# Performance work log

Measured on AMD Instinct MI355X. Metric: run time of the kernel, lower is better.

The kernel has to match this reference:

```python
import jax, jax.numpy as jnp
import numpy as np

N_NODES = 100000
N_EDGES = 1600000
IN_DIM = 64
HIDDEN_DIM = 64


def setup_inputs() -> dict:
    key = jax.random.key(0)
    ks = jax.random.split(key, 8)
    x = jax.random.normal(ks[0], (N_NODES, IN_DIM), dtype=jnp.float32)
    edge_index = jax.random.randint(ks[1], (2, N_EDGES), 0, N_NODES, dtype=jnp.int32)
    s = 1.0 / np.sqrt(IN_DIM)
    sh = 1.0 / np.sqrt(HIDDEN_DIM)
    # SAGEConv params: lin_l (applied to mean-aggregated neighbors, with bias),
    # lin_r (applied to root/self features, no bias) -- PyG defaults.
    w1l = jax.random.uniform(ks[2], (IN_DIM, HIDDEN_DIM), jnp.float32, -s, s)
    b1l = jax.random.uniform(ks[3], (HIDDEN_DIM,), jnp.float32, -s, s)
    w1r = jax.random.uniform(ks[4], (IN_DIM, HIDDEN_DIM), jnp.float32, -s, s)
    w2l = jax.random.uniform(ks[5], (HIDDEN_DIM, HIDDEN_DIM), jnp.float32, -sh, sh)
    b2l = jax.random.uniform(ks[6], (HIDDEN_DIM,), jnp.float32, -sh, sh)
    w2r = jax.random.uniform(ks[7], (HIDDEN_DIM, HIDDEN_DIM), jnp.float32, -sh, sh)
    return {"x": x, "edge_index": edge_index, "w1l": w1l, "b1l": b1l,
            "w1r": w1r, "w2l": w2l, "b2l": b2l, "w2r": w2r}


def reference(x, edge_index, w1l, b1l, w1r, w2l, b2l, w2r):
    n = x.shape[0]
    src, dst = edge_index[0], edge_index[1]
    # in-degree (number of incoming messages per target node), clamped to 1
    deg = jax.ops.segment_sum(jnp.ones(src.shape, x.dtype), dst, num_segments=n)
    inv_deg = 1.0 / jnp.maximum(deg, 1.0)  # [N]

    def sage_conv(h, wl, bl, wr):
        # mean aggregation of neighbor messages: scatter-add then normalize
        agg = jax.ops.segment_sum(h[src], dst, num_segments=n) * inv_deg[:, None]
        return agg @ wl + bl + h @ wr

    h = jax.nn.relu(sage_conv(x, w1l, b1l, w1r))  # conv1 + relu
    return sage_conv(h, w2l, b2l, w2r)            # conv2 (no activation)
```

## Files before the change

### kernel.cpp

```cpp
#include <hip/hip_runtime.h>
#include <hip/hip_fp16.h>


#define DIM 64
#define BN 64
#define MAXBUCK 2048
#define CHUNK 8192
#define GCAP 2048
#define GEMM_SMEM 12608

__device__ inline void fma4(float4& acc, float s, const float4 w) {
    acc.x = fmaf(s, w.x, acc.x); acc.y = fmaf(s, w.y, acc.y);
    acc.z = fmaf(s, w.z, acc.z); acc.w = fmaf(s, w.w, acc.w);
}

__device__ inline void addh8(float* acc, float4 raw) {
    const __half2* hp = (const __half2*)&raw;
#pragma unroll
    for (int k = 0; k < 4; ++k) {
        float2 f = __half22float2(hp[k]);
        acc[2 * k]     += f.x;
        acc[2 * k + 1] += f.y;
    }
}

__global__ __launch_bounds__(256) void prehist_kernel(const int* __restrict__ dst,
                                                      int* __restrict__ ghist,
                                                      int nE, int nbuck) {
    __shared__ int hist[MAXBUCK];
    const int t = threadIdx.x;
    for (int k = t; k < nbuck; k += 256) hist[k] = 0;
    __syncthreads();
    const int base = blockIdx.x * CHUNK;
    const int end = min(nE, base + CHUNK);
    for (int i = base + t; i < end; i += 256)
        atomicAdd(&hist[dst[i] >> 6], 1);
    __syncthreads();
    for (int k = t; k < nbuck; k += 256)
        if (hist[k]) atomicAdd(&ghist[k], hist[k]);
}

__global__ __launch_bounds__(1024) void scan_kernel(const int* __restrict__ ghist,
                                                    int* __restrict__ boff,
                                                    int* __restrict__ gcur, int nbuck) {
    __shared__ int sa[2048], sb[2048];
    const int t = threadIdx.x;
    int v0 = (t < nbuck) ? ghist[t] : 0;
    int v1 = (t + 1024 < nbuck) ? ghist[t + 1024] : 0;
    sa[t] = v0; sa[t + 1024] = v1;
    __syncthreads();
    int* in = sa; int* out = sb;
    for (int d = 1; d < 2048; d <<= 1) {
        out[t] = in[t] + ((t >= d) ? in[t - d] : 0);
        int i2 = t + 1024;
        out[i2] = in[i2] + ((i2 >= d) ? in[i2 - d] : 0);
        __syncthreads();
        int* tmp = in; in = out; out = tmp;
    }
    if (t < nbuck) { int e = in[t] - v0; boff[t] = e; gcur[t] = e; }
    if (t + 1024 < nbuck) { int e = in[t + 1024] - v1; boff[t + 1024] = e; gcur[t + 1024] = e; }
    if (t == 0) boff[nbuck] = in[2047];
}

__device__ inline void stage_rows(float* hs, const float* H, int base, int n, int t) {
    for (int p = 0; p < 4; ++p) {
        int idx = t + p * 256;
        int r = idx >> 4, c4 = idx & 15;
        int row = base + r;
        if (row < n)
            *(float4*)&hs[r * 68 + c4 * 4] = *(const float4*)&H[(size_t)row * 64 + c4 * 4];
    }
}
__device__ inline void stage_rows(float* hs, const __half* H, int base, int n, int t) {
    for (int p = 0; p < 2; ++p) {
        int idx = t + p * 256;
        int r = idx >> 3, c8 = idx & 7;
        int row = base + r;
        if (row < n) {
            float4 raw = *(const float4*)&H[(size_t)row * 64 + c8 * 8];
            const __half2* hp = (const __half2*)&raw;
            float2 f0 = __half22float2(hp[0]);
            float2 f1 = __half22float2(hp[1]);
            float2 f2 = __half22float2(hp[2]);
            float2 f3 = __half22float2(hp[3]);
            float* d = &hs[r * 68 + c8 * 8];
            *(float4*)d       = make_float4(f0.x, f0.y, f1.x, f1.y);
            *(float4*)(d + 4) = make_float4(f2.x, f2.y, f3.x, f3.y);
        }
    }
}

template <typename InT>
__device__ void gemm_body(int bid, float* smem,
                          const InT* __restrict__ H,
                          const float* __restrict__ Wl, const float* __restrict__ Wr,
                          const float* __restrict__ bias,
                          __half* __restrict__ A, __half* __restrict__ Dbuf, int n) {
    float* wsl = smem;
    float* wsr = smem + 4096;
    float* hs  = smem + 8192;
    float* bs  = smem + 8192 + 4352;
    const int t = threadIdx.x;
    for (int i = t * 4; i < 4096; i += 1024) {
        *(float4*)&wsl[i] = *(const float4*)&Wl[i];
        *(float4*)&wsr[i] = *(const float4*)&Wr[i];
    }
    if (t < 16) *(float4*)&bs[t * 4] = *(const float4*)&bias[t * 4];
    const int dg = t & 15;
    const int r0 = t >> 4;
    for (int ph = 0; ph < 2; ++ph) {
        const int base = bid * 128 + ph * 64;
        if (base >= n) break;
        __syncthreads();
        stage_rows(hs, H, base, n, t);
        __syncthreads();
        float4 accl[4] = {{0,0,0,0},{0,0,0,0},{0,0,0,0},{0,0,0,0}};
        float4 accr[4] = {{0,0,0,0},{0,0,0,0},{0,0,0,0},{0,0,0,0}};
#pragma unroll 4
        for (int kq = 0; kq < 16; ++kq) {
            float4 wl[4], wr[4];
#pragma unroll
            for (int i = 0; i < 4; ++i) {
                wl[i] = *(const float4*)&wsl[(kq * 4 + i) * 64 + dg * 4];
                wr[i] = *(const float4*)&wsr[(kq * 4 + i) * 64 + dg * 4];
            }
#pragma unroll
            for (int p = 0; p < 4; ++p) {
                float4 hv = *(const float4*)&hs[(r0 + p * 16) * 68 + kq * 4];
                fma4(accl[p], hv.x, wl[0]); fma4(accl[p], hv.y, wl[1]);
                fma4(accl[p], hv.z, wl[2]); fma4(accl[p], hv.w, wl[3]);
                fma4(accr[p], hv.x, wr[0]); fma4(accr[p], hv.y, wr[1]);
                fma4(accr[p], hv.z, wr[2]); fma4(accr[p], hv.w, wr[3]);
            }
        }
        float4 b4 = *(const float4*)&bs[dg * 4];
#pragma unroll
        for (int p = 0; p < 4; ++p) {
            int row = base + r0 + p * 16;
            if (row < n) {
                union { __half2 h[2]; float2 f; } u;
                u.h[0] = __floats2half2_rn(accl[p].x, accl[p].y);
                u.h[1] = __floats2half2_rn(accl[p].z, accl[p].w);
                *(float2*)&A[(size_t)row * 64 + dg * 4] = u.f;
                union { __half2 h[2]; float2 f; } v;
                v.h[0] = __floats2half2_rn(accr[p].x + b4.x, accr[p].y + b4.y);
                v.h[1] = __floats2half2_rn(accr[p].z + b4.z, accr[p].w + b4.w);
                *(float2*)&Dbuf[(size_t)row * 64 + dg * 4] = v.f;
            }
        }
    }
}

__global__ __launch_bounds__(256) void part_gemm_kernel(const int* __restrict__ src,
                                                        const int* __restrict__ dst,
                                                        int* __restrict__ gcur,
                                                        unsigned* __restrict__ P,
                                                        int nE, int nbuck, int pb,
                                                        const float* __restrict__ H,
                                                        const float* __restrict__ Wl,
                                                        const float* __restrict__ Wr,
                                                        const float* __restrict__ bias,
                                                        __half* __restrict__ A,
                                                        __half* __restrict__ Dbuf, int n) {
    __shared__ float smem[GEMM_SMEM];
    if ((int)blockIdx.x < pb) {
        int* hist = (int*)smem;
        const int t = threadIdx.x;
        for (int k = t; k < nbuck; k += 256) hist[k] = 0;
        __syncthreads();
        const int base = blockIdx.x * CHUNK;
        const int end = min(nE, base + CHUNK);
        for (int i = base + t; i < end; i += 256)
            atomicAdd(&hist[dst[i] >> 6], 1);
        __syncthreads();
        for (int k = t; k < nbuck; k += 256) {
            int h = hist[k];
            hist[k] = h ? atomicAdd(&gcur[k], h) : 0;
        }
        __syncthreads();
        for (int i = base + t; i < end; i += 256) {
            int d = dst[i];
            int bk = d >> 6;
            int pos = atomicAdd(&hist[bk], 1);
            P[pos] = ((unsigned)src[i] << 6) | (unsigned)(d & 63);
        }
    } else {
        gemm_body(blockIdx.x - pb, smem, H, Wl, Wr, bias, A, Dbuf, n);
    }
}

__global__ __launch_bounds__(256) void gemm_kernel(const __half* __restrict__ H,
                                                   const float* __restrict__ Wl,
                                                   const float* __restrict__ Wr,
                                                   const float* __restrict__ bias,
                                                   __half* __restrict__ A,
                                                   __half* __restrict__ Dbuf, int n) {
    __shared__ float smem[GEMM_SMEM];
    gemm_body(blockIdx.x, smem, H, Wl, Wr, bias, A, Dbuf, n);
}

template <bool RELU, typename OutT>
__global__ __launch_bounds__(256) void gather_sort_combine(const __half* __restrict__ A,
                                                           const __half* __restrict__ Dbuf,
                                                           const int* __restrict__ boff,
                                                           const unsigned* __restrict__ P,
                                                           int* __restrict__ spill,
                                                           OutT* __restrict__ out, int n) {
    __shared__ int hist[BN];
    __shared__ int rstart[BN];
    __shared__ int cur[BN];
    __shared__ int lsrc[GCAP];
    const int t = threadIdx.x;
    const int b = blockIdx.x;
    if (t < BN) hist[t] = 0;
    __syncthreads();
    const int start = boff[b], end = boff[b + 1];
    const int m = end - start;
    for (int i = start + t; i < end; i += 256)
        atomicAdd(&hist[P[i] & 63], 1);
    __syncthreads();
    if (t < 64) {
        int v = hist[t];
        int s = v;
#pragma unroll
        for (int d = 1; d < 64; d <<= 1) {
            int u = __shfl_up(s, d);
            if (t >= d) s += u;
        }
        rstart[t] = s - v;
        cur[t] = s - v;
    }
    __syncthreads();
    int* list = (m <= GCAP) ? (int*)lsrc : (spill + start);
    for (int i = start + t; i < end; i += 256) {
        unsigned p = P[i];
        int pos = atomicAdd(&cur[p & 63], 1);
        list[pos] = (int)(p >> 6);
    }
    __syncthreads();
    const int dg = t & 7;
    const size_t doff = (size_t)dg * 8;
    for (int pass = 0; pass < 2; ++pass) {
        const int r = pass * 32 + (t >> 3);
        const int node = b * BN + r;
        if (node >= n) continue;
        const int c = hist[r];
        const int* sp = list + rstart[r];
        float acc[8] = {0.f, 0.f, 0.f, 0.f, 0.f, 0.f, 0.f, 0.f};
        int j = 0;
        for (; j + 4 <= c; j += 4) {
            int e0 = sp[j + 0], e1 = sp[j + 1], e2 = sp[j + 2], e3 = sp[j + 3];
            float4 r0 = *(const float4*)&A[(size_t)e0 * 64 + doff];
            float4 r1 = *(const float4*)&A[(size_t)e1 * 64 + doff];
            float4 r2 = *(const float4*)&A[(size_t)e2 * 64 + doff];
            float4 r3 = *(const float4*)&A[(size_t)e3 * 64 + doff];
            addh8(acc, r0); addh8(acc, r1); addh8(acc, r2); addh8(acc, r3);
        }
        for (; j < c; ++j) {
            float4 rr = *(const float4*)&A[(size_t)sp[j] * 64 + doff];
            addh8(acc, rr);
        }
        const float inv = 1.0f / fmaxf((float)c, 1.0f);
        float d8[8] = {0,0,0,0,0,0,0,0};
        addh8(d8, *(const float4*)&Dbuf[(size_t)node * 64 + doff]);
        float o[8];
#pragma unroll
        for (int k = 0; k < 8; ++k) {
            float v = fmaf(acc[k], inv, d8[k]);
            o[k] = RELU ? fmaxf(v, 0.f) : v;
        }
        if constexpr (sizeof(OutT) == 2) {
            union { __half2 h[4]; float4 f; } u;
#pragma unroll
            for (int k = 0; k < 4; ++k)
                u.h[k] = __floats2half2_rn(o[2 * k], o[2 * k + 1]);
            *(float4*)&out[(size_t)node * 64 + doff] = u.f;
        } else {
            *(float4*)&out[(size_t)node * 64 + doff]     = make_float4(o[0], o[1], o[2], o[3]);
            *(float4*)&out[(size_t)node * 64 + doff + 4] = make_float4(o[4], o[5], o[6], o[7]);
        }
    }
}

extern "C" void kernel_launch(void* const* d_in, const int* in_sizes, int n_in,
                              void* d_out, int out_size, void* d_ws, size_t ws_size,
                              hipStream_t stream) {
    const float* x   = (const float*)d_in[0];
    const int*   ei  = (const int*)d_in[1];
    const float* w1l = (const float*)d_in[2];
    const float* b1l = (const float*)d_in[3];
    const float* w1r = (const float*)d_in[4];
    const float* w2l = (const float*)d_in[5];
    const float* b2l = (const float*)d_in[6];
    const float* w2r = (const float*)d_in[7];
    float* out = (float*)d_out;

    const int N = in_sizes[0] / DIM;
    const int E = in_sizes[1] / 2;
    const int* src = ei;
    const int* dst = ei + E;
    const int nbuck = (N + BN - 1) / BN;
    const int pb = (E + CHUNK - 1) / CHUNK;
    const int gb = (N + 127) / 128;

    int* ghist = (int*)d_ws;
    int* boff = ghist + nbuck;
    int* gcur = boff + nbuck + 1;
    unsigned* P = (unsigned*)(gcur + nbuck);
    int* spill = (int*)(P + E);
    uintptr_t ap = (uintptr_t)(spill + E);
    ap = (ap + 15) & ~(uintptr_t)15;
    __half* A  = (__half*)ap;
    __half* D  = A + (size_t)N * DIM;
    __half* h1 = D + (size_t)N * DIM;

    hipMemsetAsync(ghist, 0, nbuck * sizeof(int), stream);
    prehist_kernel<<<pb, 256, 0, stream>>>(dst, ghist, E, nbuck);
    scan_kernel<<<1, 1024, 0, stream>>>(ghist, boff, gcur, nbuck);
    part_gemm_kernel<<<pb + gb, 256, 0, stream>>>(src, dst, gcur, P, E, nbuck, pb,
                                                  x, w1l, w1r, b1l, A, D, N);

    gather_sort_combine<true, __half><<<nbuck, 256, 0, stream>>>(A, D, boff, P, spill, h1, N);

    gemm_kernel<<<gb, 256, 0, stream>>>(h1, w2l, w2r, b2l, A, D, N);
    gather_sort_combine<false, float><<<nbuck, 256, 0, stream>>>(A, D, boff, P, spill, out, N);
}
```

Baseline: 290.1 us.

## Replace FP32 FMA dense transform with FP16 MFMA matrix instructions

Measured after the change: 271.2 us. 6.5% less time.

```diff
diff --git a/kernel.cpp b/kernel.cpp
--- a/kernel.cpp
+++ b/kernel.cpp
@@ -7,12 +7,10 @@
 #define MAXBUCK 2048
 #define CHUNK 8192
 #define GCAP 2048
-#define GEMM_SMEM 12608
-
-__device__ inline void fma4(float4& acc, float s, const float4 w) {
-    acc.x = fmaf(s, w.x, acc.x); acc.y = fmaf(s, w.y, acc.y);
-    acc.z = fmaf(s, w.z, acc.z); acc.w = fmaf(s, w.w, acc.w);
-}
+#define WT_STRIDE 72
+
+using f16x8 = __attribute__((ext_vector_type(8))) _Float16;
+using f32x4 = __attribute__((ext_vector_type(4))) float;
 
 __device__ inline void addh8(float* acc, float4 raw) {
     const __half2* hp = (const __half2*)&raw;
@@ -62,90 +60,80 @@
     if (t == 0) boff[nbuck] = in[2047];
 }
 
-__device__ inline void stage_rows(float* hs, const float* H, int base, int n, int t) {
-    for (int p = 0; p < 4; ++p) {
-        int idx = t + p * 256;
-        int r = idx >> 4, c4 = idx & 15;
-        int row = base + r;
-        if (row < n)
-            *(float4*)&hs[r * 68 + c4 * 4] = *(const float4*)&H[(size_t)row * 64 + c4 * 4];
-    }
-}
-__device__ inline void stage_rows(float* hs, const __half* H, int base, int n, int t) {
-    for (int p = 0; p < 2; ++p) {
-        int idx = t + p * 256;
-        int r = idx >> 3, c8 = idx & 7;
-        int row = base + r;
-        if (row < n) {
-            float4 raw = *(const float4*)&H[(size_t)row * 64 + c8 * 8];
-            const __half2* hp = (const __half2*)&raw;
-            float2 f0 = __half22float2(hp[0]);
-            float2 f1 = __half22float2(hp[1]);
-            float2 f2 = __half22float2(hp[2]);
-            float2 f3 = __half22float2(hp[3]);
-            float* d = &hs[r * 68 + c8 * 8];
-            *(float4*)d       = make_float4(f0.x, f0.y, f1.x, f1.y);
-            *(float4*)(d + 4) = make_float4(f2.x, f2.y, f3.x, f3.y);
-        }
-    }
+__device__ inline void load_bfrag(const __half* __restrict__ H, long long nn, int lq,
+                                  f16x8& b0, f16x8& b1) {
+    b0 = *(const f16x8*)&H[nn * 64 + lq * 8];
+    b1 = *(const f16x8*)&H[nn * 64 + 32 + lq * 8];
+}
+__device__ inline void load_bfrag(const float* __restrict__ H, long long nn, int lq,
+                                  f16x8& b0, f16x8& b1) {
+    const float* p = &H[nn * 64 + lq * 8];
+    float4 u0 = *(const float4*)p;
+    float4 u1 = *(const float4*)(p + 4);
+    float4 u2 = *(const float4*)(p + 32);
+    float4 u3 = *(const float4*)(p + 36);
+    b0[0] = (_Float16)u0.x; b0[1] = (_Float16)u0.y; b0[2] = (_Float16)u0.z; b0[3] = (_Float16)u0.w;
+    b0[4] = (_Float16)u1.x; b0[5] = (_Float16)u1.y; b0[6] = (_Float16)u1.z; b0[7] = (_Float16)u1.w;
+    b1[0] = (_Float16)u2.x; b1[1] = (_Float16)u2.y; b1[2] = (_Float16)u2.z; b1[3] = (_Float16)u2.w;
+    b1[4] = (_Float16)u3.x; b1[5] = (_Float16)u3.y; b1[6] = (_Float16)u3.z; b1[7] = (_Float16)u3.w;
 }
 
 template <typename InT>
-__device__ void gemm_body(int bid, float* smem,
+__device__ void gemm_body(int bid, __half* wt,
                           const InT* __restrict__ H,
                           const float* __restrict__ Wl, const float* __restrict__ Wr,
                           const float* __restrict__ bias,
                           __half* __restrict__ A, __half* __restrict__ Dbuf, int n) {
-    float* wsl = smem;
-    float* wsr = smem + 4096;
-    float* hs  = smem + 8192;
-    float* bs  = smem + 8192 + 4352;
     const int t = threadIdx.x;
-    for (int i = t * 4; i < 4096; i += 1024) {
-        *(float4*)&wsl[i] = *(const float4*)&Wl[i];
-        *(float4*)&wsr[i] = *(const float4*)&Wr[i];
-    }
-    if (t < 16) *(float4*)&bs[t * 4] = *(const float4*)&bias[t * 4];
-    const int dg = t & 15;
-    const int r0 = t >> 4;
-    for (int ph = 0; ph < 2; ++ph) {
-        const int base = bid * 128 + ph * 64;
-        if (base >= n) break;
-        __syncthreads();
-        stage_rows(hs, H, base, n, t);
-        __syncthreads();
-        float4 accl[4] = {{0,0,0,0},{0,0,0,0},{0,0,0,0},{0,0,0,0}};
-        float4 accr[4] = {{0,0,0,0},{0,0,0,0},{0,0,0,0},{0,0,0,0}};
-#pragma unroll 4
-        for (int kq = 0; kq < 16; ++kq) {
-            float4 wl[4], wr[4];
-#pragma unroll
-            for (int i = 0; i < 4; ++i) {
-                wl[i] = *(const float4*)&wsl[(kq * 4 + i) * 64 + dg * 4];
-                wr[i] = *(const float4*)&wsr[(kq * 4 + i) * 64 + dg * 4];
+    for (int i = t; i < 4096; i += 256) {
+        int k = i >> 6, m = i & 63;
+        wt[(size_t)m * WT_STRIDE + k] = __float2half(Wl[i]);
+        wt[(size_t)(64 + m) * WT_STRIDE + k] = __float2half(Wr[i]);
+    }
+    __syncthreads();
+    const int lane = t & 63, wave = t >> 6;
+    const int ln = lane & 15, lq = lane >> 4;
+    f16x8 af[2][4][2];
+#pragma unroll
+    for (int mat = 0; mat < 2; ++mat)
+#pragma unroll
+        for (int mt = 0; mt < 4; ++mt)
+#pragma unroll
+            for (int ki = 0; ki < 2; ++ki)
+                af[mat][mt][ki] = *(const f16x8*)&wt[(size_t)(mat * 64 + mt * 16 + ln) * WT_STRIDE
+                                                     + ki * 32 + lq * 8];
+    float4 bf[4];
+#pragma unroll
+    for (int mt = 0; mt < 4; ++mt)
+        bf[mt] = *(const float4*)&bias[mt * 16 + lq * 4];
+
+    const int base = bid * 256;
+    for (int it = 0; it < 4; ++it) {
+        const int node = base + it * 64 + wave * 16 + ln;
+        const long long nn = (node < n) ? node : (n - 1);
+        f16x8 b0, b1;
+        load_bfrag(H, nn, lq, b0, b1);
+        f32x4 acc[2][4];
+#pragma unroll
+        for (int mat = 0; mat < 2; ++mat)
+#pragma unroll
+            for (int mt = 0; mt < 4; ++mt) {
+                f32x4 z = {0.f, 0.f, 0.f, 0.f};
+                z = __builtin_amdgcn_mfma_f32_16x16x32_f16(af[mat][mt][0], b0, z, 0, 0, 0);
+                z = __builtin_amdgcn_mfma_f32_16x16x32_f16(af[mat][mt][1], b1, z, 0, 0, 0);
+                acc[mat][mt] = z;
             }
-#pragma unroll
-            for (int p = 0; p < 4; ++p) {
-                float4 hv = *(const float4*)&hs[(r0 + p * 16) * 68 + kq * 4];
-                fma4(accl[p], hv.x, wl[0]); fma4(accl[p], hv.y, wl[1]);
-                fma4(accl[p], hv.z, wl[2]); fma4(accl[p], hv.w, wl[3]);
-                fma4(accr[p], hv.x, wr[0]); fma4(accr[p], hv.y, wr[1]);
-                fma4(accr[p], hv.z, wr[2]); fma4(accr[p], hv.w, wr[3]);
-            }
-        }
-        float4 b4 = *(const float4*)&bs[dg * 4];
-#pragma unroll
-        for (int p = 0; p < 4; ++p) {
-            int row = base + r0 + p * 16;
-            if (row < n) {
+        if (node < n) {
+#pragma unroll
+            for (int mt = 0; mt < 4; ++mt) {
                 union { __half2 h[2]; float2 f; } u;
-                u.h[0] = __floats2half2_rn(accl[p].x, accl[p].y);
-                u.h[1] = __floats2half2_rn(accl[p].z, accl[p].w);
-                *(float2*)&A[(size_t)row * 64 + dg * 4] = u.f;
+                u.h[0] = __floats2half2_rn(acc[0][mt][0], acc[0][mt][1]);
+                u.h[1] = __floats2half2_rn(acc[0][mt][2], acc[0][mt][3]);
+                *(float2*)&A[(size_t)node * 64 + mt * 16 + lq * 4] = u.f;
                 union { __half2 h[2]; float2 f; } v;
-                v.h[0] = __floats2half2_rn(accr[p].x + b4.x, accr[p].y + b4.y);
-                v.h[1] = __floats2half2_rn(accr[p].z + b4.z, accr[p].w + b4.w);
-                *(float2*)&Dbuf[(size_t)row * 64 + dg * 4] = v.f;
+                v.h[0] = __floats2half2_rn(acc[1][mt][0] + bf[mt].x, acc[1][mt][1] + bf[mt].y);
+                v.h[1] = __floats2half2_rn(acc[1][mt][2] + bf[mt].z, acc[1][mt][3] + bf[mt].w);
+                *(float2*)&Dbuf[(size_t)node * 64 + mt * 16 + lq * 4] = v.f;
             }
         }
     }
@@ -162,9 +150,9 @@
                                                         const float* __restrict__ bias,
                                                         __half* __restrict__ A,
                                                         __half* __restrict__ Dbuf, int n) {
-    __shared__ float smem[GEMM_SMEM];
+    __shared__ __align__(16) unsigned short smem_u[2 * 64 * WT_STRIDE];
     if ((int)blockIdx.x < pb) {
-        int* hist = (int*)smem;
+        int* hist = (int*)smem_u;
         const int t = threadIdx.x;
         for (int k = t; k < nbuck; k += 256) hist[k] = 0;
         __syncthreads();
@@ -185,7 +173,7 @@
             P[pos] = ((unsigned)src[i] << 6) | (unsigned)(d & 63);
         }
     } else {
-        gemm_body(blockIdx.x - pb, smem, H, Wl, Wr, bias, A, Dbuf, n);
+        gemm_body(blockIdx.x - pb, (__half*)smem_u, H, Wl, Wr, bias, A, Dbuf, n);
     }
 }
 
@@ -195,8 +183,8 @@
                                                    const float* __restrict__ bias,
                                                    __half* __restrict__ A,
                                                    __half* __restrict__ Dbuf, int n) {
-    __shared__ float smem[GEMM_SMEM];
-    gemm_body(blockIdx.x, smem, H, Wl, Wr, bias, A, Dbuf, n);
+    __shared__ __align__(16) unsigned short smem_u[2 * 64 * WT_STRIDE];
+    gemm_body(blockIdx.x, (__half*)smem_u, H, Wl, Wr, bias, A, Dbuf, n);
 }
 
 template <bool RELU, typename OutT>
@@ -261,7 +249,7 @@
             addh8(acc, rr);
         }
         const float inv = 1.0f / fmaxf((float)c, 1.0f);
-        float d8[8] = {0,0,0,0,0,0,0,0};
+        float d8[8] = {0, 0, 0, 0, 0, 0, 0, 0};
         addh8(d8, *(const float4*)&Dbuf[(size_t)node * 64 + doff]);
         float o[8];
 #pragma unroll
@@ -301,7 +289,7 @@
     const int* dst = ei + E;
     const int nbuck = (N + BN - 1) / BN;
     const int pb = (E + CHUNK - 1) / CHUNK;
-    const int gb = (N + 127) / 128;
+    const int gb = (N + 255) / 256;
 
     int* ghist = (int*)d_ws;
     int* boff = ghist + nbuck;
```
